# Performance work log

Measured on AMD Instinct MI355X. Metric: run time of the kernel, lower is better.

Reference implementation:

```python
import jax, jax.numpy as jnp
import numpy as np

N, M, K, P = 200000, 50000, 32, 15
IN_DIM, OUT_DIM = 128, 256
HID = OUT_DIM // 4
KP_EXTENT = 0.05
KP_RADIUS = 0.06
EPS = 1e-5
SLOPE = 0.1


def _lrelu(x):
    return jnp.where(x > 0, x, SLOPE * x)


def _conv1d_bn_lrelu(x, W, b, g, beta):
    # pointwise conv (1x1) + batch-norm over points + leaky relu
    x = x @ W + b
    mu = jnp.mean(x, axis=0)
    var = jnp.var(x, axis=0)
    x = (x - mu) * jax.lax.rsqrt(var + EPS) * g + beta
    return _lrelu(x)


def _kpconv_pool(points, sub_points, pools, feats, kernel_points, kp_w):
    # KPConv with strided pooling: query = sub_points [M,3], support = points [N,3]
    nbr_pts = points[pools] - sub_points[:, None, :]              # [M,K,3] relative neighbor coords
    diff = nbr_pts[:, :, None, :] - kernel_points[None, None]     # [M,K,P,3]
    dist = jnp.sqrt(jnp.sum(diff * diff, axis=-1))                # [M,K,P]
    w = jnp.maximum(0.0, 1.0 - dist / KP_EXTENT)                  # linear correlation influence
    nbr_f = feats[pools]                                          # [M,K,C]
    agg = jnp.einsum('mkp,mkc->mpc', w, nbr_f)                    # per-kernel-point aggregation
    return jnp.einsum('mpc,pcd->md', agg, kp_w)                   # [M,C_out]


def setup_inputs() -> dict:
    key = jax.random.key(0)
    ks = jax.random.split(key, 10)
    points = jax.random.uniform(ks[0], (N, 3), dtype=jnp.float32) * 0.1
    sub_points = jax.random.uniform(ks[1], (M, 3), dtype=jnp.float32) * 0.1
    features = jax.random.normal(ks[2], (N, IN_DIM), dtype=jnp.float32)
    pools = jax.random.randint(ks[3], (M, K), 0, N, dtype=jnp.int32)
    kernel_points = jax.random.uniform(ks[4], (P, 3), minval=-KP_RADIUS, maxval=KP_RADIUS, dtype=jnp.float32)
    s_in = 1.0 / np.sqrt(IN_DIM)
    s_h = 1.0 / np.sqrt(HID)
    W1 = jax.random.normal(ks[5], (IN_DIM, HID), dtype=jnp.float32) * s_in
    kp_w = jax.random.normal(ks[6], (P, HID, HID), dtype=jnp.float32) * s_h
    W2 = jax.random.normal(ks[7], (HID, OUT_DIM), dtype=jnp.float32) * s_h
    Ws = jax.random.normal(ks[8], (IN_DIM, OUT_DIM), dtype=jnp.float32) * s_in
    return dict(
        points=points, sub_points=sub_points, features=features, pools=pools,
        kernel_points=kernel_points,
        W1=W1, b1=jnp.zeros((HID,)), g1=jnp.ones((HID,)), be1=jnp.zeros((HID,)),
        kp_w=kp_w,
        W2=W2, b2=jnp.zeros((OUT_DIM,)), g2=jnp.ones((OUT_DIM,)), be2=jnp.zeros((OUT_DIM,)),
        Ws=Ws, bs=jnp.zeros((OUT_DIM,)), gs=jnp.ones((OUT_DIM,)), bes=jnp.zeros((OUT_DIM,)),
    )


def reference(points, sub_points, features, pools, kernel_points,
              W1, b1, g1, be1, kp_w, W2, b2, g2, be2, Ws, bs, gs, bes):
    # main branch: Conv1D -> KPConvPools -> leaky_relu -> Conv1D
    x = _conv1d_bn_lrelu(features, W1, b1, g1, be1)               # [N,HID]
    x = _kpconv_pool(points, sub_points, pools, x, kernel_points, kp_w)  # [M,HID]
    x = _lrelu(x)
    x = _conv1d_bn_lrelu(x, W2, b2, g2, be2)                      # [M,OUT]
    # shortcut: MaxPoolNeighbors -> Conv1D
    sc = jnp.max(features[pools], axis=1)                         # [M,IN]
    sc = _conv1d_bn_lrelu(sc, Ws, bs, gs, bes)                    # [M,OUT]
    return _lrelu(x + sc)
```

## Files before the change

kernel.cpp:

```cpp
#include <hip/hip_runtime.h>

typedef unsigned short ushort_t;
typedef unsigned int uint_t;
typedef __attribute__((ext_vector_type(8))) short bf8_t;
typedef __attribute__((ext_vector_type(4))) float f4_t;
typedef __attribute__((ext_vector_type(4))) unsigned int u4_t;

#define NPTS 200000
#define MSUB 50000
#define KNBR 32
#define PK 15
#define INDIM 128
#define OUTDIM 256
#define HID 64
#define QD2 1024
#define NB1 1563
#define NBT 1563

__device__ __forceinline__ ushort_t f2bf(float f) {
  uint_t u = __float_as_uint(f);
  u = (u + 0x7fffu + ((u >> 16) & 1u)) >> 16;
  return (ushort_t)u;
}
__device__ __forceinline__ float bf2f(ushort_t h) {
  return __uint_as_float(((uint_t)h) << 16);
}
__device__ __forceinline__ float lrelu(float x) { return fmaxf(x, 0.1f * x); }
__device__ __forceinline__ f4_t zero4() { f4_t z = {0.f, 0.f, 0.f, 0.f}; return z; }

__global__ void prep_w_kernel(const float* __restrict__ W1, const float* __restrict__ W2,
                              const float* __restrict__ Ws, const float* __restrict__ kpw,
                              ushort_t* __restrict__ W1t, ushort_t* __restrict__ W2t,
                              ushort_t* __restrict__ Wst, ushort_t* __restrict__ kpwT2) {
  const int base = blockIdx.x * blockDim.x + threadIdx.x;
  const int stride = gridDim.x * blockDim.x;
  for (int t = base; t < HID * INDIM; t += stride) {
    int c = t & 63, k = t >> 6;
    W1t[c * INDIM + k] = f2bf(W1[k * HID + c]);
  }
  for (int t = base; t < OUTDIM * HID; t += stride) {
    int c = t & 255, k = t >> 8;
    W2t[c * HID + k] = f2bf(W2[k * OUTDIM + c]);
  }
  for (int t = base; t < OUTDIM * INDIM; t += stride) {
    int c = t & 255, k = t >> 8;
    Wst[c * INDIM + k] = f2bf(Ws[k * OUTDIM + c]);
  }
  for (int t = base; t < HID * QD2; t += stride) {
    int d = t >> 10, s = t & 1023;
    int nl = s & 1, r16v = (s >> 1) & 15, gv = (s >> 5) & 3, nh = (s >> 7) & 1, rr = (s >> 8) & 3;
    int p = gv * 4 + rr, c = r16v + (nh * 2 + nl) * 16;
    float v = (p < PK) ? kpw[((long)p * HID + c) * HID + d] : 0.f;
    kpwT2[d * QD2 + s] = f2bf(v);
  }
}

__global__ __launch_bounds__(256) void conv1_kernel(const float* __restrict__ feat,
                                                    const ushort_t* __restrict__ W1t,
                                                    ushort_t* __restrict__ feat16,
                                                    ushort_t* __restrict__ x1,
                                                    float* __restrict__ part1) {
  const int tid = threadIdx.x, wid = tid >> 6, lane = tid & 63;
  const int g = lane >> 4, r16 = lane & 15;
  const int rowbase = blockIdx.x * 128 + wid * 32;
  f4_t acc[2][4];
#pragma unroll
  for (int mi = 0; mi < 2; ++mi)
#pragma unroll
    for (int ni = 0; ni < 4; ++ni) acc[mi][ni] = zero4();
#pragma unroll
  for (int kc = 0; kc < 4; ++kc) {
    const int k0 = kc * 32 + g * 8;
    bf8_t a[2], b[4];
#pragma unroll
    for (int mi = 0; mi < 2; ++mi) {
      const int row = rowbase + mi * 16 + r16;
      const int rowc = (row < NPTS) ? row : 0;
      const float4 f0 = *(const float4*)(feat + (long)rowc * INDIM + k0);
      const float4 f1 = *(const float4*)(feat + (long)rowc * INDIM + k0 + 4);
      a[mi][0] = (short)f2bf(f0.x); a[mi][1] = (short)f2bf(f0.y);
      a[mi][2] = (short)f2bf(f0.z); a[mi][3] = (short)f2bf(f0.w);
      a[mi][4] = (short)f2bf(f1.x); a[mi][5] = (short)f2bf(f1.y);
      a[mi][6] = (short)f2bf(f1.z); a[mi][7] = (short)f2bf(f1.w);
      if (row < NPTS) *(bf8_t*)(feat16 + (long)row * INDIM + k0) = a[mi];
    }
#pragma unroll
    for (int ni = 0; ni < 4; ++ni)
      b[ni] = *(const bf8_t*)(W1t + (r16 + ni * 16) * INDIM + k0);
#pragma unroll
    for (int mi = 0; mi < 2; ++mi)
#pragma unroll
      for (int ni = 0; ni < 4; ++ni)
        acc[mi][ni] = __builtin_amdgcn_mfma_f32_16x16x32_bf16(a[mi], b[ni], acc[mi][ni], 0, 0, 0);
  }
  __shared__ float red[2][64];
  if (tid < 64) { red[0][tid] = 0.f; red[1][tid] = 0.f; }
  __syncthreads();
  float cs[4] = {0.f, 0.f, 0.f, 0.f}, cq[4] = {0.f, 0.f, 0.f, 0.f};
#pragma unroll
  for (int mi = 0; mi < 2; ++mi)
#pragma unroll
    for (int rr = 0; rr < 4; ++rr) {
      const int row = rowbase + mi * 16 + g * 4 + rr;
      if (row < NPTS) {
#pragma unroll
        for (int ni = 0; ni < 4; ++ni) {
          const float v = acc[mi][ni][rr];
          cs[ni] += v;
          cq[ni] += v * v;
          x1[(long)row * HID + r16 + ni * 16] = f2bf(v);
        }
      }
    }
#pragma unroll
  for (int ni = 0; ni < 4; ++ni) {
    atomicAdd(&red[0][r16 + ni * 16], cs[ni]);
    atomicAdd(&red[1][r16 + ni * 16], cq[ni]);
  }
  __syncthreads();
  if (tid < 128) {
    const float v = (tid < 64) ? red[0][tid] : red[1][tid - 64];
    part1[(long)tid * NB1 + blockIdx.x] = v;
  }
}

__global__ __launch_bounds__(256) void reduce1fin_kernel(const float* __restrict__ part1,
                                                         const float* __restrict__ g1,
                                                         const float* __restrict__ be1,
                                                         float* __restrict__ st) {
  const int c = blockIdx.x, tid = threadIdx.x;
  const int slot = (tid < 128) ? c : (64 + c);
  const float* src = part1 + (long)slot * NB1;
  float acc = 0.f;
  for (int i = tid & 127; i < NB1; i += 128) acc += src[i];
  __shared__ float sm[256];
  sm[tid] = acc;
  __syncthreads();
  for (int s = 64; s > 0; s >>= 1) {
    if ((tid & 127) < s) sm[tid] += sm[tid + s];
    __syncthreads();
  }
  if (tid == 0) {
    const float mu = sm[0] / (float)NPTS;
    const float var = sm[128] / (float)NPTS - mu * mu;
    const float a = g1[c] * rsqrtf(var + 1e-5f);
    st[c] = a;
    st[64 + c] = be1[c] - mu * a;
  }
}

__global__ __launch_bounds__(256) void gkp_kernel(
    const float* __restrict__ points, const float* __restrict__ subp,
    const int* __restrict__ pools, const float* __restrict__ kp,
    const ushort_t* __restrict__ x1, const ushort_t* __restrict__ feat16,
    const float* __restrict__ st, const ushort_t* __restrict__ kpwT2,
    ushort_t* __restrict__ x2, ushort_t* __restrict__ scmax) {
  const int tid = threadIdx.x, wid = tid >> 6, lane = tid & 63;
  const int g = lane >> 4, r16 = lane & 15, l31 = lane & 31;
  const int mbase = blockIdx.x * 8;
  __shared__ __align__(16) char aggT[8 * 2048];
  __shared__ __align__(16) uint_t ft2[4][32][34];
  __shared__ float pts[4][32][3];
  __shared__ int idxs[4][32];
  float A4[4], S4[4];
#pragma unroll
  for (int ni = 0; ni < 4; ++ni) {
    A4[ni] = st[r16 + ni * 16];
    S4[ni] = st[64 + r16 + ni * 16];
  }
  const int p = r16;
  const int pc = (p < PK) ? p : 0;
  const float kx = kp[pc * 3 + 0], ky = kp[pc * 3 + 1], kz = kp[pc * 3 + 2];

#pragma unroll
  for (int mm = 0; mm < 2; ++mm) {
    const int lm = wid * 2 + mm;
    const int m = mbase + lm;
    if (lane < 32) idxs[wid][lane] = pools[m * KNBR + lane];
    if (lane < 32) {
      const int n = idxs[wid][lane];
      pts[wid][lane][0] = points[n * 3 + 0];
      pts[wid][lane][1] = points[n * 3 + 1];
      pts[wid][lane][2] = points[n * 3 + 2];
    }
#pragma unroll
    for (int i = 0; i < 16; ++i) {
      const int k = 2 * i + (lane >> 5);
      const int n = idxs[wid][k];
      ft2[wid][l31][k] = *(const uint_t*)(x1 + (long)n * HID + l31 * 2);
    }
    const float sx = subp[m * 3 + 0], sy = subp[m * 3 + 1], sz = subp[m * 3 + 2];
    bf8_t afrag;
#pragma unroll
    for (int j = 0; j < 8; ++j) {
      const int k = g * 8 + j;
      const float dx = pts[wid][k][0] - sx - kx;
      const float dy = pts[wid][k][1] - sy - ky;
      const float dz = pts[wid][k][2] - sz - kz;
      const float dist = sqrtf(dx * dx + dy * dy + dz * dz);
      float w = fmaxf(0.f, 1.f - dist * 20.f);
      if (p >= PK) w = 0.f;
      afrag[j] = (short)f2bf(w);
    }
    f4_t acc[4];
#pragma unroll
    for (int ni = 0; ni < 4; ++ni) acc[ni] = zero4();
#pragma unroll
    for (int ni = 0; ni < 4; ++ni) {
      const int c = r16 + ni * 16;
      const int c2 = c >> 1;
      const int sh = (c & 1) * 16;
      const float A = A4[ni], S = S4[ni];
      const uint_t* src = &ft2[wid][c2][g * 8];
      const u4_t v0 = *(const u4_t*)src;
      const u4_t v1 = *(const u4_t*)(src + 4);
      bf8_t bfrag;
#pragma unroll
      for (int j = 0; j < 4; ++j) {
        const float xa = __uint_as_float(((v0[j] >> sh) & 0xffffu) << 16);
        bfrag[j] = (short)f2bf(lrelu(A * xa + S));
        const float xb = __uint_as_float(((v1[j] >> sh) & 0xffffu) << 16);
        bfrag[4 + j] = (short)f2bf(lrelu(A * xb + S));
      }
      acc[ni] = __builtin_amdgcn_mfma_f32_16x16x32_bf16(afrag, bfrag, acc[ni], 0, 0, 0);
    }
    char* rowp = aggT + lm * 2048;
#pragma unroll
    for (int rr = 0; rr < 4; ++rr)
#pragma unroll
      for (int nh = 0; nh < 2; ++nh) {
        const uint_t v =
            (uint_t)f2bf(acc[nh * 2][rr]) | ((uint_t)f2bf(acc[nh * 2 + 1][rr]) << 16);
        int byte = ((rr * 2 + nh) * 64 + g * 16 + r16) * 4;
        byte ^= (lm & 7) << 4;
        *(uint_t*)(rowp + byte) = v;
      }
    float mx0 = -3.0e38f, mx1 = -3.0e38f;
#pragma unroll
    for (int k = 0; k < KNBR; ++k) {
      const int n = idxs[wid][k];
      const uint_t v = *(const uint_t*)(feat16 + (long)n * INDIM + lane * 2);
      mx0 = fmaxf(mx0, __uint_as_float(v << 16));
      mx1 = fmaxf(mx1, __uint_as_float(v & 0xffff0000u));
    }
    ((uint_t*)scmax)[(long)m * 64 + lane] =
        (uint_t)(__float_as_uint(mx0) >> 16) | (__float_as_uint(mx1) & 0xffff0000u);
  }
  __syncthreads();
  f4_t acc2 = zero4();
  const int arow = r16 & 7;
  const ushort_t* brow = kpwT2 + (long)(wid * 16 + r16) * QD2;
#pragma unroll 8
  for (int kc = 0; kc < 32; ++kc) {
    int byte = (kc * 64 + g * 16) ^ ((arow & 7) << 4);
    const bf8_t a = *(const bf8_t*)(aggT + arow * 2048 + byte);
    const bf8_t b = *(const bf8_t*)(brow + kc * 32 + g * 8);
    acc2 = __builtin_amdgcn_mfma_f32_16x16x32_bf16(a, b, acc2, 0, 0, 0);
  }
  if (g < 2) {
#pragma unroll
    for (int rr = 0; rr < 4; ++rr) {
      const int m = mbase + g * 4 + rr;
      x2[(long)m * HID + wid * 16 + r16] = f2bf(lrelu(acc2[rr]));
    }
  }
}

template <int KD>
__device__ __forceinline__ void convT_body(const ushort_t* __restrict__ A,
                                           const ushort_t* __restrict__ Bt,
                                           ushort_t* __restrict__ Oraw,
                                           float* __restrict__ part, int blk) {
  const int tid = threadIdx.x, lane = tid & 63;
  const int wid = tid >> 6;
  const int g = lane >> 4, r16 = lane & 15;
  const int rowbase = blk * 32;
  const int colbase = wid * 64;
  f4_t acc[2][4];
#pragma unroll
  for (int mi = 0; mi < 2; ++mi)
#pragma unroll
    for (int ni = 0; ni < 4; ++ni) acc[mi][ni] = zero4();
#pragma unroll
  for (int kc = 0; kc < KD / 32; ++kc) {
    const int k0 = kc * 32 + g * 8;
    bf8_t a[2], b[4];
#pragma unroll
    for (int mi = 0; mi < 2; ++mi) {
      int row = rowbase + mi * 16 + r16;
      if (row >= MSUB) row = 0;
      a[mi] = *(const bf8_t*)(A + (long)row * KD + k0);
    }
#pragma unroll
    for (int ni = 0; ni < 4; ++ni)
      b[ni] = *(const bf8_t*)(Bt + (long)(colbase + r16 + ni * 16) * KD + k0);
#pragma unroll
    for (int mi = 0; mi < 2; ++mi)
#pragma unroll
      for (int ni = 0; ni < 4; ++ni)
        acc[mi][ni] = __builtin_amdgcn_mfma_f32_16x16x32_bf16(a[mi], b[ni], acc[mi][ni], 0, 0, 0);
  }
  __shared__ float red[2][256];
  red[0][tid] = 0.f;
  red[1][tid] = 0.f;
  __syncthreads();
  float cs[4] = {0.f, 0.f, 0.f, 0.f}, cq[4] = {0.f, 0.f, 0.f, 0.f};
#pragma unroll
  for (int mi = 0; mi < 2; ++mi)
#pragma unroll
    for (int rr = 0; rr < 4; ++rr) {
      const int row = rowbase + mi * 16 + g * 4 + rr;
      if (row < MSUB) {
#pragma unroll
        for (int ni = 0; ni < 4; ++ni) {
          const float v = acc[mi][ni][rr];
          cs[ni] += v;
          cq[ni] += v * v;
          Oraw[(long)row * OUTDIM + colbase + r16 + ni * 16] = f2bf(v);
        }
      }
    }
#pragma unroll
  for (int ni = 0; ni < 4; ++ni) {
    atomicAdd(&red[0][colbase + r16 + ni * 16], cs[ni]);
    atomicAdd(&red[1][colbase + r16 + ni * 16], cq[ni]);
  }
  __syncthreads();
  part[(long)tid * NBT + blk] = red[0][tid];
  part[(long)(256 + tid) * NBT + blk] = red[1][tid];
}

__global__ __launch_bounds__(256) void convT_merged_kernel(
    const ushort_t* __restrict__ x2, const ushort_t* __restrict__ W2t,
    const ushort_t* __restrict__ scmax, const ushort_t* __restrict__ Wst,
    ushort_t* __restrict__ x3, ushort_t* __restrict__ scraw,
    float* __restrict__ part2, float* __restrict__ part3) {
  const int b = blockIdx.x;
  if (b < NBT)
    convT_body<HID>(x2, W2t, x3, part2, b);
  else
    convT_body<INDIM>(scmax, Wst, scraw, part3, b - NBT);
}

__global__ __launch_bounds__(256) void reduce23fin_kernel(const float* __restrict__ part2,
                                                          const float* __restrict__ part3,
                                                          const float* __restrict__ g2,
                                                          const float* __restrict__ be2,
                                                          const float* __restrict__ gs,
                                                          const float* __restrict__ bes,
                                                          float* __restrict__ st) {
  const int blk = blockIdx.x, tid = threadIdx.x;
  const int sc = blk >> 8, c = blk & 255;
  const float* part = sc ? part3 : part2;
  const int slot = (tid < 128) ? c : (256 + c);
  const float* src = part + (long)slot * NBT;
  float acc = 0.f;
  for (int i = tid & 127; i < NBT; i += 128) acc += src[i];
  __shared__ float sm[256];
  sm[tid] = acc;
  __syncthreads();
  for (int s = 64; s > 0; s >>= 1) {
    if ((tid & 127) < s) sm[tid] += sm[tid + s];
    __syncthreads();
  }
  if (tid == 0) {
    const float mu = sm[0] / (float)MSUB;
    const float var = sm[128] / (float)MSUB - mu * mu;
    const float a = (sc ? gs : g2)[c] * rsqrtf(var + 1e-5f);
    const int off = sc ? 640 : 128;
    st[off + c] = a;
    st[off + 256 + c] = (sc ? bes : be2)[c] - mu * a;
  }
}

__global__ __launch_bounds__(256) void final_kernel(const ushort_t* __restrict__ x3,
                                                    const ushort_t* __restrict__ sc,
                                                    const float* __restrict__ st,
                                                    float* __restrict__ out) {
  const int i = blockIdx.x * 256 + threadIdx.x;
  const int c0 = (i * 4) & 255;
  const uint2 xv = ((const uint2*)x3)[i];
  const uint2 sv = ((const uint2*)sc)[i];
  float xs[4] = {bf2f((ushort_t)(xv.x & 0xffffu)), bf2f((ushort_t)(xv.x >> 16)),
                 bf2f((ushort_t)(xv.y & 0xffffu)), bf2f((ushort_t)(xv.y >> 16))};
  float ss[4] = {bf2f((ushort_t)(sv.x & 0xffffu)), bf2f((ushort_t)(sv.x >> 16)),
                 bf2f((ushort_t)(sv.y & 0xffffu)), bf2f((ushort_t)(sv.y >> 16))};
  float r[4];
#pragma unroll
  for (int j = 0; j < 4; ++j) {
    const int c = c0 + j;
    const float v = lrelu(st[128 + c] * xs[j] + st[384 + c]);
    const float u = lrelu(st[640 + c] * ss[j] + st[896 + c]);
    r[j] = lrelu(v + u);
  }
  ((float4*)out)[i] = make_float4(r[0], r[1], r[2], r[3]);
}

extern "C" void kernel_launch(void* const* d_in, const int* in_sizes, int n_in,
                              void* d_out, int out_size, void* d_ws, size_t ws_size,
                              hipStream_t stream) {
  (void)in_sizes; (void)n_in; (void)out_size;
  const float* points = (const float*)d_in[0];
  const float* subp = (const float*)d_in[1];
  const float* feat = (const float*)d_in[2];
  const int* pools = (const int*)d_in[3];
  const float* kp = (const float*)d_in[4];
  const float* W1 = (const float*)d_in[5];
  const float* g1 = (const float*)d_in[7];
  const float* be1 = (const float*)d_in[8];
  const float* kpw = (const float*)d_in[9];
  const float* W2 = (const float*)d_in[10];
  const float* g2 = (const float*)d_in[12];
  const float* be2 = (const float*)d_in[13];
  const float* Wsm = (const float*)d_in[14];
  const float* gs = (const float*)d_in[16];
  const float* bes = (const float*)d_in[17];
  float* out = (float*)d_out;

  char* w = (char*)d_ws;
  size_t o = 0;
  ushort_t* feat16 = (ushort_t*)(w + o); o += (size_t)NPTS * INDIM * 2;
  ushort_t* x1 = (ushort_t*)(w + o);     o += (size_t)NPTS * HID * 2;
  ushort_t* x2 = (ushort_t*)(w + o);     o += (size_t)MSUB * HID * 2;
  ushort_t* x3 = (ushort_t*)(w + o);     o += (size_t)MSUB * OUTDIM * 2;
  ushort_t* scmax = (ushort_t*)(w + o);  o += (size_t)MSUB * INDIM * 2;
  ushort_t* scraw = (ushort_t*)(w + o);  o += (size_t)MSUB * OUTDIM * 2;
  float* part1 = (float*)(w + o);        o += (size_t)128 * NB1 * 4;
  float* part2 = (float*)(w + o);        o += (size_t)512 * NBT * 4;
  float* part3 = (float*)(w + o);        o += (size_t)512 * NBT * 4;
  ushort_t* W1t = (ushort_t*)(w + o);    o += HID * INDIM * 2;
  ushort_t* W2t = (ushort_t*)(w + o);    o += OUTDIM * HID * 2;
  ushort_t* Wst = (ushort_t*)(w + o);    o += OUTDIM * INDIM * 2;
  ushort_t* kpwT2 = (ushort_t*)(w + o);  o += HID * QD2 * 2;
  float* st = (float*)(w + o);           o += 1152 * 4;
  if (ws_size < o) return;

  prep_w_kernel<<<64, 256, 0, stream>>>(W1, W2, Wsm, kpw, W1t, W2t, Wst, kpwT2);
  conv1_kernel<<<NB1, 256, 0, stream>>>(feat, W1t, feat16, x1, part1);
  reduce1fin_kernel<<<64, 256, 0, stream>>>(part1, g1, be1, st);
  gkp_kernel<<<MSUB / 8, 256, 0, stream>>>(points, subp, pools, kp, x1, feat16, st,
                                           kpwT2, x2, scmax);
  convT_merged_kernel<<<2 * NBT, 256, 0, stream>>>(x2, W2t, scmax, Wst, x3, scraw,
                                                   part2, part3);
  reduce23fin_kernel<<<512, 256, 0, stream>>>(part2, part3, g2, be2, gs, bes, st);
  final_kernel<<<MSUB * OUTDIM / 1024, 256, 0, stream>>>(x3, scraw, st, out);
}
```

Baseline: 297.8 us.

## Split fused gather/KPConv kernel into gather-aggregate and separate kernel-point GEMM

The fused gather+KPConv kernel becomes two kernels. The first gathers neighbours and computes per-kernel-point aggregates, one subpoint per wave, with no block-level sync. It uses shuffles instead of shared staging for indices and coordinates, and 16-byte vectorized loads for both the feature gather and the max-pool. The aggregates are written to a global buffer, and a second kernel runs the [M,1024]x[1024,64] GEMM with each wave computing a 16x64 tile. This should raise occupancy and memory-level parallelism, at the cost of writing and rereading about 100MB of aggregates. Workspace buffers are aliased (x2 reuses x1, the partials share the aggregate region) to keep the footprint in check.

```diff
diff --git a/kernel.cpp b/kernel.cpp
--- a/kernel.cpp
+++ b/kernel.cpp
@@ -149,119 +149,143 @@
   }
 }
 
-__global__ __launch_bounds__(256) void gkp_kernel(
+__global__ __launch_bounds__(256, 8) void gather_kernel(
     const float* __restrict__ points, const float* __restrict__ subp,
     const int* __restrict__ pools, const float* __restrict__ kp,
     const ushort_t* __restrict__ x1, const ushort_t* __restrict__ feat16,
-    const float* __restrict__ st, const ushort_t* __restrict__ kpwT2,
-    ushort_t* __restrict__ x2, ushort_t* __restrict__ scmax) {
+    const float* __restrict__ st, ushort_t* __restrict__ agg2,
+    ushort_t* __restrict__ scmax) {
   const int tid = threadIdx.x, wid = tid >> 6, lane = tid & 63;
-  const int g = lane >> 4, r16 = lane & 15, l31 = lane & 31;
-  const int mbase = blockIdx.x * 8;
-  __shared__ __align__(16) char aggT[8 * 2048];
-  __shared__ __align__(16) uint_t ft2[4][32][34];
-  __shared__ float pts[4][32][3];
-  __shared__ int idxs[4][32];
+  const int g = lane >> 4, r16 = lane & 15;
+  const int m = blockIdx.x * 4 + wid;
+  __shared__ __align__(16) uint_t ft2[4][32][36];
+  const int idx0 = pools[m * KNBR + (lane & 31)];
+  float px = 0.f, py = 0.f, pz = 0.f;
+  if (lane < 32) {
+    px = points[idx0 * 3 + 0];
+    py = points[idx0 * 3 + 1];
+    pz = points[idx0 * 3 + 2];
+  }
   float A4[4], S4[4];
 #pragma unroll
   for (int ni = 0; ni < 4; ++ni) {
     A4[ni] = st[r16 + ni * 16];
     S4[ni] = st[64 + r16 + ni * 16];
   }
+  const float sx = subp[m * 3 + 0], sy = subp[m * 3 + 1], sz = subp[m * 3 + 2];
+  const int krow = lane >> 3, cb = lane & 7;
+#pragma unroll
+  for (int it = 0; it < 4; ++it) {
+    const int k = it * 8 + krow;
+    const int n = __shfl(idx0, k);
+    const u4_t v = *(const u4_t*)(x1 + (long)n * HID + cb * 8);
+#pragma unroll
+    for (int j = 0; j < 4; ++j) ft2[wid][cb * 4 + j][k] = v[j];
+  }
   const int p = r16;
   const int pc = (p < PK) ? p : 0;
-  const float kx = kp[pc * 3 + 0], ky = kp[pc * 3 + 1], kz = kp[pc * 3 + 2];
-
-#pragma unroll
-  for (int mm = 0; mm < 2; ++mm) {
-    const int lm = wid * 2 + mm;
-    const int m = mbase + lm;
-    if (lane < 32) idxs[wid][lane] = pools[m * KNBR + lane];
-    if (lane < 32) {
-      const int n = idxs[wid][lane];
-      pts[wid][lane][0] = points[n * 3 + 0];
-      pts[wid][lane][1] = points[n * 3 + 1];
-      pts[wid][lane][2] = points[n * 3 + 2];
-    }
-#pragma unroll
-    for (int i = 0; i < 16; ++i) {
-      const int k = 2 * i + (lane >> 5);
-      const int n = idxs[wid][k];
-      ft2[wid][l31][k] = *(const uint_t*)(x1 + (long)n * HID + l31 * 2);
-    }
-    const float sx = subp[m * 3 + 0], sy = subp[m * 3 + 1], sz = subp[m * 3 + 2];
-    bf8_t afrag;
-#pragma unroll
-    for (int j = 0; j < 8; ++j) {
-      const int k = g * 8 + j;
-      const float dx = pts[wid][k][0] - sx - kx;
-      const float dy = pts[wid][k][1] - sy - ky;
-      const float dz = pts[wid][k][2] - sz - kz;
-      const float dist = sqrtf(dx * dx + dy * dy + dz * dz);
-      float w = fmaxf(0.f, 1.f - dist * 20.f);
-      if (p >= PK) w = 0.f;
-      afrag[j] = (short)f2bf(w);
-    }
-    f4_t acc[4];
-#pragma unroll
-    for (int ni = 0; ni < 4; ++ni) acc[ni] = zero4();
-#pragma unroll
-    for (int ni = 0; ni < 4; ++ni) {
-      const int c = r16 + ni * 16;
-      const int c2 = c >> 1;
-      const int sh = (c & 1) * 16;
-      const float A = A4[ni], S = S4[ni];
-      const uint_t* src = &ft2[wid][c2][g * 8];
-      const u4_t v0 = *(const u4_t*)src;
-      const u4_t v1 = *(const u4_t*)(src + 4);
-      bf8_t bfrag;
-#pragma unroll
-      for (int j = 0; j < 4; ++j) {
-        const float xa = __uint_as_float(((v0[j] >> sh) & 0xffffu) << 16);
-        bfrag[j] = (short)f2bf(lrelu(A * xa + S));
-        const float xb = __uint_as_float(((v1[j] >> sh) & 0xffffu) << 16);
-        bfrag[4 + j] = (short)f2bf(lrelu(A * xb + S));
-      }
-      acc[ni] = __builtin_amdgcn_mfma_f32_16x16x32_bf16(afrag, bfrag, acc[ni], 0, 0, 0);
-    }
-    char* rowp = aggT + lm * 2048;
-#pragma unroll
-    for (int rr = 0; rr < 4; ++rr)
-#pragma unroll
-      for (int nh = 0; nh < 2; ++nh) {
-        const uint_t v =
-            (uint_t)f2bf(acc[nh * 2][rr]) | ((uint_t)f2bf(acc[nh * 2 + 1][rr]) << 16);
-        int byte = ((rr * 2 + nh) * 64 + g * 16 + r16) * 4;
-        byte ^= (lm & 7) << 4;
-        *(uint_t*)(rowp + byte) = v;
-      }
-    float mx0 = -3.0e38f, mx1 = -3.0e38f;
-#pragma unroll
-    for (int k = 0; k < KNBR; ++k) {
-      const int n = idxs[wid][k];
-      const uint_t v = *(const uint_t*)(feat16 + (long)n * INDIM + lane * 2);
-      mx0 = fmaxf(mx0, __uint_as_float(v << 16));
-      mx1 = fmaxf(mx1, __uint_as_float(v & 0xffff0000u));
-    }
-    ((uint_t*)scmax)[(long)m * 64 + lane] =
-        (uint_t)(__float_as_uint(mx0) >> 16) | (__float_as_uint(mx1) & 0xffff0000u);
-  }
-  __syncthreads();
-  f4_t acc2 = zero4();
-  const int arow = r16 & 7;
-  const ushort_t* brow = kpwT2 + (long)(wid * 16 + r16) * QD2;
-#pragma unroll 8
+  const float kxx = kp[pc * 3 + 0] + sx, kyy = kp[pc * 3 + 1] + sy, kzz = kp[pc * 3 + 2] + sz;
+  bf8_t afrag;
+#pragma unroll
+  for (int j = 0; j < 8; ++j) {
+    const int k = g * 8 + j;
+    const float dx = __shfl(px, k) - kxx;
+    const float dy = __shfl(py, k) - kyy;
+    const float dz = __shfl(pz, k) - kzz;
+    const float dist = sqrtf(dx * dx + dy * dy + dz * dz);
+    float w = fmaxf(0.f, 1.f - dist * 20.f);
+    if (p >= PK) w = 0.f;
+    afrag[j] = (short)f2bf(w);
+  }
+  f4_t acc[4];
+#pragma unroll
+  for (int ni = 0; ni < 4; ++ni) acc[ni] = zero4();
+#pragma unroll
+  for (int ni = 0; ni < 4; ++ni) {
+    const int c = r16 + ni * 16;
+    const int c2 = c >> 1;
+    const int sh = (c & 1) * 16;
+    const float A = A4[ni], S = S4[ni];
+    const uint_t* src = &ft2[wid][c2][g * 8];
+    const u4_t v0 = *(const u4_t*)src;
+    const u4_t v1 = *(const u4_t*)(src + 4);
+    bf8_t bfrag;
+#pragma unroll
+    for (int j = 0; j < 4; ++j) {
+      const float xa = __uint_as_float(((v0[j] >> sh) & 0xffffu) << 16);
+      bfrag[j] = (short)f2bf(lrelu(A * xa + S));
+      const float xb = __uint_as_float(((v1[j] >> sh) & 0xffffu) << 16);
+      bfrag[4 + j] = (short)f2bf(lrelu(A * xb + S));
+    }
+    acc[ni] = __builtin_amdgcn_mfma_f32_16x16x32_bf16(afrag, bfrag, acc[ni], 0, 0, 0);
+  }
+  uint_t* aggu = (uint_t*)(agg2 + (long)m * QD2);
+#pragma unroll
+  for (int rr = 0; rr < 4; ++rr)
+#pragma unroll
+    for (int nh = 0; nh < 2; ++nh) {
+      const uint_t v = (uint_t)f2bf(acc[nh * 2][rr]) | ((uint_t)f2bf(acc[nh * 2 + 1][rr]) << 16);
+      aggu[(rr * 2 + nh) * 64 + g * 16 + r16] = v;
+    }
+  const int kr2 = lane >> 4, cb2 = lane & 15;
+  float mx[8];
+#pragma unroll
+  for (int j = 0; j < 8; ++j) mx[j] = -3.0e38f;
+#pragma unroll
+  for (int it = 0; it < 8; ++it) {
+    const int k = it * 4 + kr2;
+    const int n = __shfl(idx0, k);
+    const u4_t v = *(const u4_t*)(feat16 + (long)n * INDIM + cb2 * 8);
+#pragma unroll
+    for (int j = 0; j < 4; ++j) {
+      mx[2 * j] = fmaxf(mx[2 * j], __uint_as_float(v[j] << 16));
+      mx[2 * j + 1] = fmaxf(mx[2 * j + 1], __uint_as_float(v[j] & 0xffff0000u));
+    }
+  }
+#pragma unroll
+  for (int j = 0; j < 8; ++j) {
+    mx[j] = fmaxf(mx[j], __shfl_xor(mx[j], 16));
+    mx[j] = fmaxf(mx[j], __shfl_xor(mx[j], 32));
+  }
+  if (lane < 16) {
+    u4_t o;
+#pragma unroll
+    for (int j = 0; j < 4; ++j)
+      o[j] = (__float_as_uint(mx[2 * j]) >> 16) | (__float_as_uint(mx[2 * j + 1]) & 0xffff0000u);
+    *(u4_t*)(scmax + (long)m * INDIM + lane * 8) = o;
+  }
+}
+
+__global__ __launch_bounds__(256) void kpgemm_kernel(const ushort_t* __restrict__ agg2,
+                                                     const ushort_t* __restrict__ kpwT2,
+                                                     ushort_t* __restrict__ x2) {
+  const int tid = threadIdx.x, wid = tid >> 6, lane = tid & 63;
+  const int g = lane >> 4, r16 = lane & 15;
+  const int rowbase = blockIdx.x * 64 + wid * 16;
+  f4_t acc[4];
+#pragma unroll
+  for (int ni = 0; ni < 4; ++ni) acc[ni] = zero4();
+  int arow = rowbase + r16;
+  if (arow >= MSUB) arow = 0;
+  const ushort_t* aptr = agg2 + (long)arow * QD2;
   for (int kc = 0; kc < 32; ++kc) {
-    int byte = (kc * 64 + g * 16) ^ ((arow & 7) << 4);
-    const bf8_t a = *(const bf8_t*)(aggT + arow * 2048 + byte);
-    const bf8_t b = *(const bf8_t*)(brow + kc * 32 + g * 8);
-    acc2 = __builtin_amdgcn_mfma_f32_16x16x32_bf16(a, b, acc2, 0, 0, 0);
-  }
-  if (g < 2) {
-#pragma unroll
-    for (int rr = 0; rr < 4; ++rr) {
-      const int m = mbase + g * 4 + rr;
-      x2[(long)m * HID + wid * 16 + r16] = f2bf(lrelu(acc2[rr]));
+    const int k0 = kc * 32 + g * 8;
+    const bf8_t a = *(const bf8_t*)(aptr + k0);
+    bf8_t b[4];
+#pragma unroll
+    for (int ni = 0; ni < 4; ++ni)
+      b[ni] = *(const bf8_t*)(kpwT2 + (long)(r16 + ni * 16) * QD2 + k0);
+#pragma unroll
+    for (int ni = 0; ni < 4; ++ni)
+      acc[ni] = __builtin_amdgcn_mfma_f32_16x16x32_bf16(a, b[ni], acc[ni], 0, 0, 0);
+  }
+#pragma unroll
+  for (int rr = 0; rr < 4; ++rr) {
+    const int row = rowbase + g * 4 + rr;
+    if (row < MSUB) {
+#pragma unroll
+      for (int ni = 0; ni < 4; ++ni)
+        x2[(long)row * HID + r16 + ni * 16] = f2bf(lrelu(acc[ni][rr]));
     }
   }
 }
@@ -421,25 +445,28 @@
   size_t o = 0;
   ushort_t* feat16 = (ushort_t*)(w + o); o += (size_t)NPTS * INDIM * 2;
   ushort_t* x1 = (ushort_t*)(w + o);     o += (size_t)NPTS * HID * 2;
-  ushort_t* x2 = (ushort_t*)(w + o);     o += (size_t)MSUB * HID * 2;
-  ushort_t* x3 = (ushort_t*)(w + o);     o += (size_t)MSUB * OUTDIM * 2;
   ushort_t* scmax = (ushort_t*)(w + o);  o += (size_t)MSUB * INDIM * 2;
-  ushort_t* scraw = (ushort_t*)(w + o);  o += (size_t)MSUB * OUTDIM * 2;
-  float* part1 = (float*)(w + o);        o += (size_t)128 * NB1 * 4;
-  float* part2 = (float*)(w + o);        o += (size_t)512 * NBT * 4;
-  float* part3 = (float*)(w + o);        o += (size_t)512 * NBT * 4;
+  char* aggbase = w + o;                 o += (size_t)MSUB * QD2 * 2;
   ushort_t* W1t = (ushort_t*)(w + o);    o += HID * INDIM * 2;
   ushort_t* W2t = (ushort_t*)(w + o);    o += OUTDIM * HID * 2;
   ushort_t* Wst = (ushort_t*)(w + o);    o += OUTDIM * INDIM * 2;
   ushort_t* kpwT2 = (ushort_t*)(w + o);  o += HID * QD2 * 2;
   float* st = (float*)(w + o);           o += 1152 * 4;
   if (ws_size < o) return;
+  float* part1 = (float*)aggbase;
+  ushort_t* agg2 = (ushort_t*)aggbase;
+  ushort_t* x3 = (ushort_t*)aggbase;
+  ushort_t* scraw = (ushort_t*)(aggbase + (size_t)MSUB * OUTDIM * 2);
+  float* part2 = (float*)(aggbase + (size_t)2 * MSUB * OUTDIM * 2);
+  float* part3 = (float*)(aggbase + (size_t)2 * MSUB * OUTDIM * 2 + (size_t)512 * NBT * 4);
+  ushort_t* x2 = x1;
 
   prep_w_kernel<<<64, 256, 0, stream>>>(W1, W2, Wsm, kpw, W1t, W2t, Wst, kpwT2);
   conv1_kernel<<<NB1, 256, 0, stream>>>(feat, W1t, feat16, x1, part1);
   reduce1fin_kernel<<<64, 256, 0, stream>>>(part1, g1, be1, st);
-  gkp_kernel<<<MSUB / 8, 256, 0, stream>>>(points, subp, pools, kp, x1, feat16, st,
-                                           kpwT2, x2, scmax);
+  gather_kernel<<<MSUB / 4, 256, 0, stream>>>(points, subp, pools, kp, x1, feat16, st,
+                                              agg2, scmax);
+  kpgemm_kernel<<<(MSUB + 63) / 64, 256, 0, stream>>>(agg2, kpwT2, x2);
   convT_merged_kernel<<<2 * NBT, 256, 0, stream>>>(x2, W2t, scmax, Wst, x3, scraw,
                                                    part2, part3);
   reduce23fin_kernel<<<512, 256, 0, stream>>>(part2, part3, g2, be2, gs, bes, st);
```

Result: slower. 338.3 us (+13.6%).
